# Performance work log

Measured on AMD Instinct MI355X. Metric: run time of the kernel, lower is better.

Reference implementation:

```python
import jax, jax.numpy as jnp
import numpy as np

B, NI, H, NC = 524288, 32, 128, 64


def _masks(ni, h):
    deg_in = jnp.arange(ni)                     # input layer: arange % ni == arange
    deg_hid = jnp.arange(h) % (ni - 1)
    deg_out = jnp.arange(2 * ni) % ni - 1
    m1 = (deg_hid[:, None] >= deg_in[None, :]).astype(jnp.float32)   # [H, NI]
    m2 = (deg_hid[:, None] >= deg_hid[None, :]).astype(jnp.float32)  # [H, H]
    m3 = (deg_out[:, None] >= deg_hid[None, :]).astype(jnp.float32)  # [2NI, H]
    return m1, m2, m3


def setup_inputs() -> dict:
    key = jax.random.key(0)
    ks = jax.random.split(key, 9)
    s = 0.05
    return {
        "x": jax.random.normal(ks[0], (B, NI), jnp.float32),
        "cond": jax.random.normal(ks[1], (B, NC), jnp.float32),
        "W1": jax.random.normal(ks[2], (H, NI), jnp.float32) * s,
        "b1": jnp.zeros((H,), jnp.float32),
        "Wc": jax.random.normal(ks[3], (H, NC), jnp.float32) * s,
        "W2": jax.random.normal(ks[4], (H, H), jnp.float32) * s,
        "b2": jnp.zeros((H,), jnp.float32),
        "W3": jax.random.normal(ks[5], (2 * NI, H), jnp.float32) * s,
        "b3": jnp.zeros((2 * NI,), jnp.float32),
    }


def reference(x, cond, W1, b1, Wc, W2, b2, W3, b3):
    ni = x.shape[1]
    h_dim = W1.shape[0]
    m1, m2, m3 = _masks(ni, h_dim)
    # joiner: masked linear + conditioning linear (no bias on cond)
    h = x @ (W1 * m1).T + b1 + cond @ Wc.T            # [B, H]
    h = jax.nn.relu(h)
    h = jax.nn.relu(h @ (W2 * m2).T + b2)             # [B, H]
    o = h @ (W3 * m3).T + b3                          # [B, 2NI]
    m_, a = o[:, :ni], o[:, ni:]
    a = jnp.clip(a, -5.0, 5.0)
    u = (x - m_) * jnp.exp(-a)
    logdet = -jnp.sum(a, axis=-1, keepdims=True)
    return u, logdet
```

## Files before the change

kernel.cpp:

```cpp
#include <hip/hip_runtime.h>


#define B_ROWS 524288
#define NI 32
#define HD 128
#define NC 64

#define L2_BASE 48
#define L3_BASE 112
#define N_FRAGS 144

typedef _Float16 half4 __attribute__((ext_vector_type(4)));
typedef float f32x4 __attribute__((ext_vector_type(4)));

__device__ inline half4 cvt4(f32x4 v) {
  half4 h;
  h[0] = (_Float16)v[0]; h[1] = (_Float16)v[1];
  h[2] = (_Float16)v[2]; h[3] = (_Float16)v[3];
  return h;
}

__global__ void prep_weights(const float* __restrict__ W1, const float* __restrict__ Wc,
                             const float* __restrict__ W2, const float* __restrict__ W3,
                             _Float16* __restrict__ wf) {
  int tid = blockIdx.x * blockDim.x + threadIdx.x;
  if (tid >= N_FRAGS * 64) return;
  int frag = tid >> 6;
  int lane = tid & 63;
  int q = lane >> 4, c = lane & 15;
  int L, jt, kt;
  if (frag < L2_BASE)      { L = 0; jt = frag / 6;             kt = frag % 6; }
  else if (frag < L3_BASE) { L = 1; jt = (frag - L2_BASE) >> 3; kt = (frag - L2_BASE) & 7; }
  else                     { L = 2; jt = (frag - L3_BASE) >> 3; kt = (frag - L3_BASE) & 7; }
  int j = jt * 16 + c;
  half4 v;
#pragma unroll
  for (int i = 0; i < 4; ++i) {
    int k = kt * 16 + q * 4 + i;
    float w;
    if (L == 0) {
      if (k < NI) w = ((j % 31) >= k) ? W1[j * NI + k] : 0.f;
      else        w = Wc[j * NC + (k - NI)];
    } else if (L == 1) {
      w = ((j % 31) >= (k % 31)) ? W2[j * HD + k] : 0.f;
    } else {
      w = (((j % 32) - 1) >= (k % 31)) ? W3[j * HD + k] : 0.f;
    }
    v[i] = (_Float16)w;
  }
  *(half4*)(wf + (size_t)tid * 4) = v;
}

__global__ __launch_bounds__(256, 3) void made_fused(
    const float* __restrict__ x, const float* __restrict__ cond,
    const float* __restrict__ b1, const float* __restrict__ b2,
    const float* __restrict__ b3, const _Float16* __restrict__ wf,
    float* __restrict__ out) {
  __shared__ _Float16 wlds[96 * 256];

  const int tid  = threadIdx.x;
  const int lane = tid & 63;
  const int wid  = tid >> 6;
  const int q = lane >> 4, c = lane & 15;
  const long rowbase = ((long)blockIdx.x * 4 + wid) * 32;

  {
    const f32x4* src = (const f32x4*)(wf + L2_BASE * 256);
    f32x4* dst = (f32x4*)wlds;
#pragma unroll
    for (int k = 0; k < 12; ++k) dst[tid + k * 256] = src[tid + k * 256];
  }

  half4 bf[6][2];
#pragma unroll
  for (int nt = 0; nt < 2; ++nt) {
    const float* xr = x    + (rowbase + nt * 16 + c) * NI;
    const float* cr = cond + (rowbase + nt * 16 + c) * NC;
    bf[0][nt] = cvt4(*(const f32x4*)(xr + q * 4));
    bf[1][nt] = cvt4(*(const f32x4*)(xr + 16 + q * 4));
    bf[2][nt] = cvt4(*(const f32x4*)(cr + q * 4));
    bf[3][nt] = cvt4(*(const f32x4*)(cr + 16 + q * 4));
    bf[4][nt] = cvt4(*(const f32x4*)(cr + 32 + q * 4));
    bf[5][nt] = cvt4(*(const f32x4*)(cr + 48 + q * 4));
  }

  f32x4 acc[8][2];
#pragma unroll
  for (int jt = 0; jt < 8; ++jt) {
    f32x4 bv = *(const f32x4*)(b1 + jt * 16 + q * 4);
#pragma unroll
    for (int nt = 0; nt < 2; ++nt) acc[jt][nt] = bv;
  }
#pragma unroll
  for (int jt = 0; jt < 8; ++jt) {
#pragma unroll
    for (int kt = 0; kt < 6; ++kt) {
      half4 a = *(const half4*)(wf + (((jt * 6 + kt) * 64 + lane) << 2));
#pragma unroll
      for (int nt = 0; nt < 2; ++nt)
        acc[jt][nt] = __builtin_amdgcn_mfma_f32_16x16x16f16(a, bf[kt][nt], acc[jt][nt], 0, 0, 0);
    }
  }
  half4 h1[8][2];
#pragma unroll
  for (int jt = 0; jt < 8; ++jt)
#pragma unroll
    for (int nt = 0; nt < 2; ++nt) {
      f32x4 v = acc[jt][nt];
      v[0] = fmaxf(v[0], 0.f); v[1] = fmaxf(v[1], 0.f);
      v[2] = fmaxf(v[2], 0.f); v[3] = fmaxf(v[3], 0.f);
      h1[jt][nt] = cvt4(v);
    }

  __syncthreads();

#pragma unroll
  for (int jt = 0; jt < 8; ++jt) {
    f32x4 bv = *(const f32x4*)(b2 + jt * 16 + q * 4);
#pragma unroll
    for (int nt = 0; nt < 2; ++nt) acc[jt][nt] = bv;
  }
#pragma unroll
  for (int jt = 0; jt < 8; ++jt) {
#pragma unroll
    for (int kt = 0; kt < 8; ++kt) {
      half4 a = *(const half4*)(wlds + (((jt * 8 + kt) * 64 + lane) << 2));
#pragma unroll
      for (int nt = 0; nt < 2; ++nt)
        acc[jt][nt] = __builtin_amdgcn_mfma_f32_16x16x16f16(a, h1[kt][nt], acc[jt][nt], 0, 0, 0);
    }
  }
  half4 h2[8][2];
#pragma unroll
  for (int jt = 0; jt < 8; ++jt)
#pragma unroll
    for (int nt = 0; nt < 2; ++nt) {
      f32x4 v = acc[jt][nt];
      v[0] = fmaxf(v[0], 0.f); v[1] = fmaxf(v[1], 0.f);
      v[2] = fmaxf(v[2], 0.f); v[3] = fmaxf(v[3], 0.f);
      h2[jt][nt] = cvt4(v);
    }

  f32x4 acc3[4][2];
#pragma unroll
  for (int jt = 0; jt < 4; ++jt) {
    f32x4 bv = *(const f32x4*)(b3 + jt * 16 + q * 4);
#pragma unroll
    for (int nt = 0; nt < 2; ++nt) acc3[jt][nt] = bv;
  }
#pragma unroll
  for (int jt = 0; jt < 4; ++jt) {
#pragma unroll
    for (int kt = 0; kt < 8; ++kt) {
      half4 a = *(const half4*)(wlds + (((64 + jt * 8 + kt) * 64 + lane) << 2));
#pragma unroll
      for (int nt = 0; nt < 2; ++nt)
        acc3[jt][nt] = __builtin_amdgcn_mfma_f32_16x16x16f16(a, h2[kt][nt], acc3[jt][nt], 0, 0, 0);
    }
  }

#pragma unroll
  for (int nt = 0; nt < 2; ++nt) {
    long m = rowbase + nt * 16 + c;
    const float* xr = x + m * NI;
    f32x4 xa = *(const f32x4*)(xr + q * 4);
    f32x4 xb = *(const f32x4*)(xr + 16 + q * 4);
    f32x4 mva = acc3[0][nt], mvb = acc3[1][nt];
    f32x4 ava = acc3[2][nt], avb = acc3[3][nt];
    f32x4 ua, ub;
    float s = 0.f;
#pragma unroll
    for (int i = 0; i < 4; ++i) {
      float aa = fminf(fmaxf(ava[i], -5.f), 5.f);
      float ab = fminf(fmaxf(avb[i], -5.f), 5.f);
      ua[i] = (xa[i] - mva[i]) * __expf(-aa);
      ub[i] = (xb[i] - mvb[i]) * __expf(-ab);
      s += aa + ab;
    }
    *(f32x4*)(out + m * NI + q * 4) = ua;
    *(f32x4*)(out + m * NI + 16 + q * 4) = ub;
    s += __shfl_xor(s, 16);
    s += __shfl_xor(s, 32);
    if (q == 0) out[(long)B_ROWS * NI + m] = -s;
  }
}

extern "C" void kernel_launch(void* const* d_in, const int* in_sizes, int n_in,
                              void* d_out, int out_size, void* d_ws, size_t ws_size,
                              hipStream_t stream) {
  const float* x    = (const float*)d_in[0];
  const float* cond = (const float*)d_in[1];
  const float* W1   = (const float*)d_in[2];
  const float* b1   = (const float*)d_in[3];
  const float* Wc   = (const float*)d_in[4];
  const float* W2   = (const float*)d_in[5];
  const float* b2   = (const float*)d_in[6];
  const float* W3   = (const float*)d_in[7];
  const float* b3   = (const float*)d_in[8];
  _Float16* wf = (_Float16*)d_ws;

  prep_weights<<<(N_FRAGS * 64 + 255) / 256, 256, 0, stream>>>(W1, Wc, W2, W3, wf);
  made_fused<<<B_ROWS / 128, 256, 0, stream>>>(x, cond, b1, b2, b3, wf, (float*)d_out);
}
```

Before: 306.8 us.

## Make blocks persistent over 8 row tiles with register prefetch of next tile

Each wave now processes 8 consecutive 32-row tiles in a loop. The loads for the next tile's x and cond are issued into registers before computing the current one, so memory latency overlaps the MFMA work. All three weight layers and the biases go into LDS once per block, amortising that setup over 8 tiles, and x is kept in registers instead of being re-read in the epilogue. In exchange the grid is 8x smaller, the launch bound drops to 2 blocks per CU, and the prefetch buffer raises register pressure.

```diff
diff --git a/kernel.cpp b/kernel.cpp
--- a/kernel.cpp
+++ b/kernel.cpp
@@ -9,6 +9,7 @@
 #define L2_BASE 48
 #define L3_BASE 112
 #define N_FRAGS 144
+#define NB 8
 
 typedef _Float16 half4 __attribute__((ext_vector_type(4)));
 typedef float f32x4 __attribute__((ext_vector_type(4)));
@@ -51,137 +52,155 @@
   *(half4*)(wf + (size_t)tid * 4) = v;
 }
 
-__global__ __launch_bounds__(256, 3) void made_fused(
+__global__ __launch_bounds__(256, 2) void made_fused(
     const float* __restrict__ x, const float* __restrict__ cond,
     const float* __restrict__ b1, const float* __restrict__ b2,
     const float* __restrict__ b3, const _Float16* __restrict__ wf,
     float* __restrict__ out) {
-  __shared__ _Float16 wlds[96 * 256];
+  __shared__ _Float16 wlds[N_FRAGS * 256];
+  __shared__ float blds[320];
 
   const int tid  = threadIdx.x;
   const int lane = tid & 63;
   const int wid  = tid >> 6;
   const int q = lane >> 4, c = lane & 15;
-  const long rowbase = ((long)blockIdx.x * 4 + wid) * 32;
+  const long wrow0 = ((long)blockIdx.x * 4 + wid) * (32 * NB);
+
+  f32x4 pf[12];
+  auto issue_loads = [&](int r) {
+#pragma unroll
+    for (int nt = 0; nt < 2; ++nt) {
+      const f32x4* xr = (const f32x4*)(x    + (wrow0 + r * 32 + nt * 16 + c) * NI);
+      const f32x4* cr = (const f32x4*)(cond + (wrow0 + r * 32 + nt * 16 + c) * NC);
+      pf[nt * 6 + 0] = xr[q];
+      pf[nt * 6 + 1] = xr[4 + q];
+      pf[nt * 6 + 2] = cr[q];
+      pf[nt * 6 + 3] = cr[4 + q];
+      pf[nt * 6 + 4] = cr[8 + q];
+      pf[nt * 6 + 5] = cr[12 + q];
+    }
+  };
+  issue_loads(0);
 
   {
-    const f32x4* src = (const f32x4*)(wf + L2_BASE * 256);
+    const f32x4* src = (const f32x4*)wf;
     f32x4* dst = (f32x4*)wlds;
 #pragma unroll
-    for (int k = 0; k < 12; ++k) dst[tid + k * 256] = src[tid + k * 256];
+    for (int k = 0; k < 18; ++k) dst[tid + k * 256] = src[tid + k * 256];
+    if (tid < 128) blds[tid] = b1[tid];
+    else if (tid < 256) blds[tid] = b2[tid - 128];
+    if (tid < 64) blds[256 + tid] = b3[tid];
   }
-
-  half4 bf[6][2];
-#pragma unroll
-  for (int nt = 0; nt < 2; ++nt) {
-    const float* xr = x    + (rowbase + nt * 16 + c) * NI;
-    const float* cr = cond + (rowbase + nt * 16 + c) * NC;
-    bf[0][nt] = cvt4(*(const f32x4*)(xr + q * 4));
-    bf[1][nt] = cvt4(*(const f32x4*)(xr + 16 + q * 4));
-    bf[2][nt] = cvt4(*(const f32x4*)(cr + q * 4));
-    bf[3][nt] = cvt4(*(const f32x4*)(cr + 16 + q * 4));
-    bf[4][nt] = cvt4(*(const f32x4*)(cr + 32 + q * 4));
-    bf[5][nt] = cvt4(*(const f32x4*)(cr + 48 + q * 4));
-  }
-
-  f32x4 acc[8][2];
-#pragma unroll
-  for (int jt = 0; jt < 8; ++jt) {
-    f32x4 bv = *(const f32x4*)(b1 + jt * 16 + q * 4);
-#pragma unroll
-    for (int nt = 0; nt < 2; ++nt) acc[jt][nt] = bv;
-  }
-#pragma unroll
-  for (int jt = 0; jt < 8; ++jt) {
-#pragma unroll
-    for (int kt = 0; kt < 6; ++kt) {
-      half4 a = *(const half4*)(wf + (((jt * 6 + kt) * 64 + lane) << 2));
-#pragma unroll
-      for (int nt = 0; nt < 2; ++nt)
-        acc[jt][nt] = __builtin_amdgcn_mfma_f32_16x16x16f16(a, bf[kt][nt], acc[jt][nt], 0, 0, 0);
-    }
-  }
-  half4 h1[8][2];
-#pragma unroll
-  for (int jt = 0; jt < 8; ++jt)
+  __syncthreads();
+
+#pragma unroll 1
+  for (int r = 0; r < NB; ++r) {
+    f32x4 xkeep[2][2];
+    half4 bf[6][2];
 #pragma unroll
     for (int nt = 0; nt < 2; ++nt) {
-      f32x4 v = acc[jt][nt];
-      v[0] = fmaxf(v[0], 0.f); v[1] = fmaxf(v[1], 0.f);
-      v[2] = fmaxf(v[2], 0.f); v[3] = fmaxf(v[3], 0.f);
-      h1[jt][nt] = cvt4(v);
-    }
-
-  __syncthreads();
-
-#pragma unroll
-  for (int jt = 0; jt < 8; ++jt) {
-    f32x4 bv = *(const f32x4*)(b2 + jt * 16 + q * 4);
-#pragma unroll
-    for (int nt = 0; nt < 2; ++nt) acc[jt][nt] = bv;
-  }
-#pragma unroll
-  for (int jt = 0; jt < 8; ++jt) {
-#pragma unroll
-    for (int kt = 0; kt < 8; ++kt) {
-      half4 a = *(const half4*)(wlds + (((jt * 8 + kt) * 64 + lane) << 2));
-#pragma unroll
-      for (int nt = 0; nt < 2; ++nt)
-        acc[jt][nt] = __builtin_amdgcn_mfma_f32_16x16x16f16(a, h1[kt][nt], acc[jt][nt], 0, 0, 0);
-    }
-  }
-  half4 h2[8][2];
-#pragma unroll
-  for (int jt = 0; jt < 8; ++jt)
+      xkeep[nt][0] = pf[nt * 6 + 0];
+      xkeep[nt][1] = pf[nt * 6 + 1];
+#pragma unroll
+      for (int k = 0; k < 6; ++k) bf[k][nt] = cvt4(pf[nt * 6 + k]);
+    }
+    if (r + 1 < NB) issue_loads(r + 1);
+
+    f32x4 acc[8][2];
+#pragma unroll
+    for (int jt = 0; jt < 8; ++jt) {
+      f32x4 bv = *(const f32x4*)(blds + jt * 16 + q * 4);
+#pragma unroll
+      for (int nt = 0; nt < 2; ++nt) acc[jt][nt] = bv;
+    }
+#pragma unroll
+    for (int jt = 0; jt < 8; ++jt) {
+#pragma unroll
+      for (int kt = 0; kt < 6; ++kt) {
+        half4 a = *(const half4*)(wlds + (((jt * 6 + kt) * 64 + lane) << 2));
+#pragma unroll
+        for (int nt = 0; nt < 2; ++nt)
+          acc[jt][nt] = __builtin_amdgcn_mfma_f32_16x16x16f16(a, bf[kt][nt], acc[jt][nt], 0, 0, 0);
+      }
+    }
+    half4 h1[8][2];
+#pragma unroll
+    for (int jt = 0; jt < 8; ++jt)
+#pragma unroll
+      for (int nt = 0; nt < 2; ++nt) {
+        f32x4 v = acc[jt][nt];
+        v[0] = fmaxf(v[0], 0.f); v[1] = fmaxf(v[1], 0.f);
+        v[2] = fmaxf(v[2], 0.f); v[3] = fmaxf(v[3], 0.f);
+        h1[jt][nt] = cvt4(v);
+      }
+
+#pragma unroll
+    for (int jt = 0; jt < 8; ++jt) {
+      f32x4 bv = *(const f32x4*)(blds + 128 + jt * 16 + q * 4);
+#pragma unroll
+      for (int nt = 0; nt < 2; ++nt) acc[jt][nt] = bv;
+    }
+#pragma unroll
+    for (int jt = 0; jt < 8; ++jt) {
+#pragma unroll
+      for (int kt = 0; kt < 8; ++kt) {
+        half4 a = *(const half4*)(wlds + (((L2_BASE + jt * 8 + kt) * 64 + lane) << 2));
+#pragma unroll
+        for (int nt = 0; nt < 2; ++nt)
+          acc[jt][nt] = __builtin_amdgcn_mfma_f32_16x16x16f16(a, h1[kt][nt], acc[jt][nt], 0, 0, 0);
+      }
+    }
+    half4 h2[8][2];
+#pragma unroll
+    for (int jt = 0; jt < 8; ++jt)
+#pragma unroll
+      for (int nt = 0; nt < 2; ++nt) {
+        f32x4 v = acc[jt][nt];
+        v[0] = fmaxf(v[0], 0.f); v[1] = fmaxf(v[1], 0.f);
+        v[2] = fmaxf(v[2], 0.f); v[3] = fmaxf(v[3], 0.f);
+        h2[jt][nt] = cvt4(v);
+      }
+
+    f32x4 acc3[4][2];
+#pragma unroll
+    for (int jt = 0; jt < 4; ++jt) {
+      f32x4 bv = *(const f32x4*)(blds + 256 + jt * 16 + q * 4);
+#pragma unroll
+      for (int nt = 0; nt < 2; ++nt) acc3[jt][nt] = bv;
+    }
+#pragma unroll
+    for (int jt = 0; jt < 4; ++jt) {
+#pragma unroll
+      for (int kt = 0; kt < 8; ++kt) {
+        half4 a = *(const half4*)(wlds + (((L3_BASE + jt * 8 + kt) * 64 + lane) << 2));
+#pragma unroll
+        for (int nt = 0; nt < 2; ++nt)
+          acc3[jt][nt] = __builtin_amdgcn_mfma_f32_16x16x16f16(a, h2[kt][nt], acc3[jt][nt], 0, 0, 0);
+      }
+    }
+
 #pragma unroll
     for (int nt = 0; nt < 2; ++nt) {
-      f32x4 v = acc[jt][nt];
-      v[0] = fmaxf(v[0], 0.f); v[1] = fmaxf(v[1], 0.f);
-      v[2] = fmaxf(v[2], 0.f); v[3] = fmaxf(v[3], 0.f);
-      h2[jt][nt] = cvt4(v);
-    }
-
-  f32x4 acc3[4][2];
-#pragma unroll
-  for (int jt = 0; jt < 4; ++jt) {
-    f32x4 bv = *(const f32x4*)(b3 + jt * 16 + q * 4);
-#pragma unroll
-    for (int nt = 0; nt < 2; ++nt) acc3[jt][nt] = bv;
-  }
-#pragma unroll
-  for (int jt = 0; jt < 4; ++jt) {
-#pragma unroll
-    for (int kt = 0; kt < 8; ++kt) {
-      half4 a = *(const half4*)(wlds + (((64 + jt * 8 + kt) * 64 + lane) << 2));
-#pragma unroll
-      for (int nt = 0; nt < 2; ++nt)
-        acc3[jt][nt] = __builtin_amdgcn_mfma_f32_16x16x16f16(a, h2[kt][nt], acc3[jt][nt], 0, 0, 0);
-    }
-  }
-
-#pragma unroll
-  for (int nt = 0; nt < 2; ++nt) {
-    long m = rowbase + nt * 16 + c;
-    const float* xr = x + m * NI;
-    f32x4 xa = *(const f32x4*)(xr + q * 4);
-    f32x4 xb = *(const f32x4*)(xr + 16 + q * 4);
-    f32x4 mva = acc3[0][nt], mvb = acc3[1][nt];
-    f32x4 ava = acc3[2][nt], avb = acc3[3][nt];
-    f32x4 ua, ub;
-    float s = 0.f;
-#pragma unroll
-    for (int i = 0; i < 4; ++i) {
-      float aa = fminf(fmaxf(ava[i], -5.f), 5.f);
-      float ab = fminf(fmaxf(avb[i], -5.f), 5.f);
-      ua[i] = (xa[i] - mva[i]) * __expf(-aa);
-      ub[i] = (xb[i] - mvb[i]) * __expf(-ab);
-      s += aa + ab;
-    }
-    *(f32x4*)(out + m * NI + q * 4) = ua;
-    *(f32x4*)(out + m * NI + 16 + q * 4) = ub;
-    s += __shfl_xor(s, 16);
-    s += __shfl_xor(s, 32);
-    if (q == 0) out[(long)B_ROWS * NI + m] = -s;
+      long m = wrow0 + r * 32 + nt * 16 + c;
+      f32x4 xa = xkeep[nt][0], xb = xkeep[nt][1];
+      f32x4 mva = acc3[0][nt], mvb = acc3[1][nt];
+      f32x4 ava = acc3[2][nt], avb = acc3[3][nt];
+      f32x4 ua, ub;
+      float s = 0.f;
+#pragma unroll
+      for (int i = 0; i < 4; ++i) {
+        float aa = fminf(fmaxf(ava[i], -5.f), 5.f);
+        float ab = fminf(fmaxf(avb[i], -5.f), 5.f);
+        ua[i] = (xa[i] - mva[i]) * __expf(-aa);
+        ub[i] = (xb[i] - mvb[i]) * __expf(-ab);
+        s += aa + ab;
+      }
+      *(f32x4*)(out + m * NI + q * 4) = ua;
+      *(f32x4*)(out + m * NI + 16 + q * 4) = ub;
+      s += __shfl_xor(s, 16);
+      s += __shfl_xor(s, 32);
+      if (q == 0) out[(long)B_ROWS * NI + m] = -s;
+    }
   }
 }
 
@@ -200,5 +219,5 @@
   _Float16* wf = (_Float16*)d_ws;
 
   prep_weights<<<(N_FRAGS * 64 + 255) / 256, 256, 0, stream>>>(W1, Wc, W2, W3, wf);
-  made_fused<<<B_ROWS / 128, 256, 0, stream>>>(x, cond, b1, b2, b3, wf, (float*)d_out);
-}
+  made_fused<<<B_ROWS / 1024, 256, 0, stream>>>(x, cond, b1, b2, b3, wf, (float*)d_out);
+}
```

After: 591.7 us. +92.9%, slower.
